# Performance work log

Hardware: AMD Instinct MI355X
Metric: run time of the kernel (lower is better)

Reference implementation:

```python
import jax, jax.numpy as jnp
import numpy as np

D_MODEL, D_KEY, N_HEADS = 256, 32, 8
B, T1, T2 = 4, 2048, 2048


def setup_inputs() -> dict:
    key = jax.random.key(0)
    ks = jax.random.split(key, 12)
    s = 1.0 / np.sqrt(D_MODEL)
    inp = {
        "key_input": jax.random.normal(ks[0], (B, T1, D_MODEL), jnp.float32),
        "query_input": jax.random.normal(ks[1], (B, T2, D_MODEL), jnp.float32),
        "value_input": jax.random.normal(ks[2], (B, T1, D_MODEL), jnp.float32),
        "attention_mask": jnp.ones((B, T1, T2), dtype=jnp.bool_),  # unused by the module, kept for API fidelity
        "WK_w": jax.random.uniform(ks[3], (D_KEY * N_HEADS, D_MODEL), jnp.float32, -s, s),
        "WK_b": jax.random.uniform(ks[4], (D_KEY * N_HEADS,), jnp.float32, -s, s),
        "WQ_w": jax.random.uniform(ks[5], (D_KEY * N_HEADS, D_MODEL), jnp.float32, -s, s),
        "WQ_b": jax.random.uniform(ks[6], (D_KEY * N_HEADS,), jnp.float32, -s, s),
        "WV_w": jax.random.uniform(ks[7], (D_MODEL * N_HEADS, D_MODEL), jnp.float32, -s, s),
        "WV_b": jax.random.uniform(ks[8], (D_MODEL * N_HEADS,), jnp.float32, -s, s),
        "WO_w": jax.random.uniform(ks[9], (D_MODEL, D_MODEL * N_HEADS), jnp.float32, -1.0 / np.sqrt(D_MODEL * N_HEADS), 1.0 / np.sqrt(D_MODEL * N_HEADS)),
        "WO_b": jax.random.uniform(ks[10], (D_MODEL,), jnp.float32, -1.0 / np.sqrt(D_MODEL * N_HEADS), 1.0 / np.sqrt(D_MODEL * N_HEADS)),
    }
    return inp


def reference(key_input, query_input, value_input, attention_mask,
              WK_w, WK_b, WQ_w, WQ_b, WV_w, WV_b, WO_w, WO_b):
    b, t1, dm = key_input.shape
    t2 = query_input.shape[1]
    h, dk = N_HEADS, D_KEY
    # projections
    k = key_input @ WK_w.T + WK_b      # [b, t1, h*dk]
    q = query_input @ WQ_w.T + WQ_b    # [b, t2, h*dk]
    v = value_input @ WV_w.T + WV_b    # [b, t1, h*dm] (per-head value dim == d_model)
    # head split: channel index c = head*dk + feat (head outer), matching torch reshapes
    k = k.reshape(b, t1, h, dk)
    q = q.reshape(b, t2, h, dk)
    v = v.reshape(b, t1, h, dm)
    # scores: NO 1/sqrt(dk) scaling and NO masking (faithful to source; mask arg unused)
    scores = jnp.einsum('bshk,bqhk->bhsq', k, q)      # [b, h, t1, t2]
    attn = jax.nn.softmax(scores, axis=2)             # softmax over KEY axis (torch dim=1 of [t1,t2])
    emb = jnp.einsum('bshd,bhsq->bqdh', v, attn)      # [b, t2, dm, h]
    emb = emb.reshape(b, t2, dm * h)                  # flatten (d_model outer, head inner)
    return emb @ WO_w.T + WO_b                        # [b, t2, d_model]
```

## Files before the change

### kernel.cpp

```cpp
#include <hip/hip_runtime.h>

typedef __attribute__((ext_vector_type(8))) short short8;
typedef __attribute__((ext_vector_type(4))) short short4v;
typedef __attribute__((ext_vector_type(4))) float float4v;
typedef __attribute__((ext_vector_type(4))) unsigned uint4v;
typedef __attribute__((ext_vector_type(2))) unsigned uint2v;
typedef __attribute__((ext_vector_type(4))) _Float16 half4;

constexpr int T  = 2048;
constexpr int DM = 256;
constexpr int DK = 32;

__device__ inline short f2bf(float f) {
  unsigned u = __builtin_bit_cast(unsigned, f);
  u += 0x7fff + ((u >> 16) & 1);
  return (short)(u >> 16);
}

__device__ inline unsigned pk2(float a, float b) {
#if __has_builtin(__builtin_amdgcn_cvt_pk_bf16_f32)
  auto r = __builtin_amdgcn_cvt_pk_bf16_f32(a, b);
  return __builtin_bit_cast(unsigned, r);
#else
  unsigned ua = __builtin_bit_cast(unsigned, a);
  ua = (ua + 0x7fff + ((ua >> 16) & 1)) >> 16;
  unsigned ub = __builtin_bit_cast(unsigned, b);
  ub = (ub + 0x7fff + ((ub >> 16) & 1)) >> 16;
  return ua | (ub << 16);
#endif
}

__device__ inline float fexp2(float x) {
#if __has_builtin(__builtin_amdgcn_exp2f)
  return __builtin_amdgcn_exp2f(x);
#else
  return exp2f(x);
#endif
}

__device__ inline short8 load8_bf(const float* __restrict__ p) {
  float4v a = *(const float4v*)p;
  float4v b = *(const float4v*)(p + 4);
  uint4v u;
  u[0] = pk2(a[0], a[1]); u[1] = pk2(a[2], a[3]);
  u[2] = pk2(b[0], b[1]); u[3] = pk2(b[2], b[3]);
  return __builtin_bit_cast(short8, u);
}

__device__ inline void gemm_body64(const float* __restrict__ A,
                                   const float* __restrict__ Bw,
                                   const float* __restrict__ bias,
                                   short* __restrict__ C,
                                   float oscale, int bx, int by,
                                   int K, int N,
                                   short (&As)[128][40], short (&Bs)[64][40]) {
  const int tid  = threadIdx.x;
  const int wave = tid >> 6, lane = tid & 63;
  const int l15  = lane & 15, quad = lane >> 4;
  const int wm   = (wave & 1) * 64, wn = (wave >> 1) * 32;
  const long Abase = (long)bx * 128;
  const long Bbase = (long)by * 64;

  float4v acc[4][2];
  for (int i = 0; i < 4; i++)
    for (int j = 0; j < 2; j++)
      for (int r = 0; r < 4; r++) acc[i][j][r] = 0.f;

  const int srow = tid >> 2;
  const int sc8  = (tid & 3) * 8;

  for (int k0 = 0; k0 < K; k0 += 32) {
    __syncthreads();
    for (int i = 0; i < 2; i++) {
      int row = srow + i * 64;
      *(short8*)&As[row][sc8] = load8_bf(A + (Abase + row) * K + k0 + sc8);
    }
    *(short8*)&Bs[srow][sc8] = load8_bf(Bw + (Bbase + srow) * K + k0 + sc8);
    __syncthreads();
    short8 af[4], bfr[2];
    for (int ms = 0; ms < 4; ms++) af[ms]  = *(const short8*)&As[wm + ms*16 + l15][quad*8];
    for (int ns = 0; ns < 2; ns++) bfr[ns] = *(const short8*)&Bs[wn + ns*16 + l15][quad*8];
    for (int ms = 0; ms < 4; ms++)
      for (int ns = 0; ns < 2; ns++)
        acc[ms][ns] = __builtin_amdgcn_mfma_f32_16x16x32_bf16(af[ms], bfr[ns], acc[ms][ns], 0, 0, 0);
  }

  for (int ms = 0; ms < 4; ms++) {
    int rowl = wm + ms*16 + quad*4;
    for (int ns = 0; ns < 2; ns++) {
      int col = (int)Bbase + wn + ns*16 + l15;
      float bv = bias[col];
      for (int r = 0; r < 4; r++) {
        long row = Abase + rowl + r;
        C[row * (long)N + col] = f2bf((acc[ms][ns][r] + bv) * oscale);
      }
    }
  }
}

__global__ __launch_bounds__(256)
void prep(const float* __restrict__ key_x, const float* __restrict__ query_x,
          const float* __restrict__ WK_w, const float* __restrict__ WK_b,
          const float* __restrict__ WQ_w, const float* __restrict__ WQ_b,
          const float* __restrict__ WV_w, const float* __restrict__ WV_b,
          const float* __restrict__ WO_w,
          short* __restrict__ Kp, short* __restrict__ Qp,
          short* __restrict__ Wf, float* __restrict__ cbias) {
  __shared__ __align__(16) short As[128][40];
  __shared__ __align__(16) short Bs[64][40];
  __shared__ float cb_s[16][17];

  const int gb  = blockIdx.x;
  const int tid = threadIdx.x;

  if (gb < 512) {
    const int g = gb & 255;
    const int bx = g & 63, by = g >> 6;
    if (gb < 256)
      gemm_body64(key_x,   WK_w, WK_b, Kp, 1.0f,        bx, by, 256, 256, As, Bs);
    else
      gemm_body64(query_x, WQ_w, WQ_b, Qp, 1.44269504f, bx, by, 256, 256, As, Bs);
  } else if (gb < 576) {
    const int w  = gb - 512;
    const int h  = w >> 3;
    const int bx = (w >> 2) & 1;
    const int by = w & 3;
    const int wave = tid >> 6, lane = tid & 63;
    const int l15  = lane & 15, quad = lane >> 4;
    const int wm   = (wave & 1) * 64, wn = (wave >> 1) * 32;
    const int srow = tid >> 2, sc8 = (tid & 3) * 8;

    float4v acc[4][2];
    for (int i = 0; i < 4; i++)
      for (int j = 0; j < 2; j++)
        for (int r = 0; r < 4; r++) acc[i][j][r] = 0.f;

    for (int d0 = 0; d0 < 256; d0 += 32) {
      __syncthreads();
      for (int i = 0; i < 2; i++) {
        int row = srow + i * 64;
        for (int j = 0; j < 8; j++)
          As[row][sc8 + j] = f2bf(WO_w[(bx*128 + row) * 2048 + (d0 + sc8 + j) * 8 + h]);
      }
      for (int j = 0; j < 8; j++)
        Bs[srow][sc8 + j] = f2bf(WV_w[((h*256) + d0 + sc8 + j) * 256 + by*64 + srow]);
      __syncthreads();
      short8 af[4], bfr[2];
      for (int ms = 0; ms < 4; ms++) af[ms]  = *(const short8*)&As[wm + ms*16 + l15][quad*8];
      for (int ns = 0; ns < 2; ns++) bfr[ns] = *(const short8*)&Bs[wn + ns*16 + l15][quad*8];
      for (int ms = 0; ms < 4; ms++)
        for (int ns = 0; ns < 2; ns++)
          acc[ms][ns] = __builtin_amdgcn_mfma_f32_16x16x32_bf16(af[ms], bfr[ns], acc[ms][ns], 0, 0, 0);
    }
    for (int ms = 0; ms < 4; ms++) {
      int m = bx*128 + wm + ms*16 + quad*4;
      for (int ns = 0; ns < 2; ns++) {
        int col = by*64 + wn + ns*16 + l15;
        for (int r = 0; r < 4; r++)
          Wf[((long)h*256 + m + r) * 256 + col] = f2bf(acc[ms][ns][r]);
      }
    }
  } else {
    const int idx = gb - 576;
    const int h = idx >> 4, ng = idx & 15;
    const int ni = tid & 15, di = tid >> 4;
    const int n = ng * 16 + ni;
    float acc = 0.f;
    for (int j = 0; j < 16; j++) {
      int d = di * 16 + j;
      acc += WV_b[h*256 + d] * WO_w[n * 2048 + d*8 + h];
    }
    cb_s[ni][di] = acc;
    __syncthreads();
    if (tid < 16) {
      float s = 0.f;
      for (int d2 = 0; d2 < 16; d2++) s += cb_s[tid][d2];
      cbias[h*256 + ng*16 + tid] = s;
    }
  }
}

__global__ __launch_bounds__(256)
void gemm_ut(const short* __restrict__ Wf, const float* __restrict__ Bw,
             const float* __restrict__ cbias, short* __restrict__ Ut) {
  __shared__ __align__(16) short As[128][40];
  __shared__ __align__(16) short Bs[128][40];

  const int tid  = threadIdx.x;
  const int wave = tid >> 6, lane = tid & 63;
  const int l15  = lane & 15, quad = lane >> 4;
  const int wm   = (wave & 1) * 64, wn = (wave >> 1) * 64;
  const long Abase = (long)blockIdx.x * 128;
  const long Bbase = (long)blockIdx.y * 128;

  float4v acc[4][4];
  for (int i = 0; i < 4; i++)
    for (int j = 0; j < 4; j++)
      for (int r = 0; r < 4; r++) acc[i][j][r] = 0.f;

  const int srow = tid >> 2;
  const int sc8  = (tid & 3) * 8;

  for (int k0 = 0; k0 < 256; k0 += 32) {
    __syncthreads();
    for (int i = 0; i < 2; i++) {
      int row = srow + i * 64;
      *(short8*)&As[row][sc8] = *(const short8*)(Wf + (Abase + row) * 256 + k0 + sc8);
      *(short8*)&Bs[row][sc8] = load8_bf(Bw + (Bbase + row) * 256 + k0 + sc8);
    }
    __syncthreads();
    short8 af[4], bfr[4];
    for (int ms = 0; ms < 4; ms++) af[ms]  = *(const short8*)&As[wm + ms*16 + l15][quad*8];
    for (int ns = 0; ns < 4; ns++) bfr[ns] = *(const short8*)&Bs[wn + ns*16 + l15][quad*8];
    for (int ms = 0; ms < 4; ms++)
      for (int ns = 0; ns < 4; ns++)
        acc[ms][ns] = __builtin_amdgcn_mfma_f32_16x16x32_bf16(af[ms], bfr[ns], acc[ms][ns], 0, 0, 0);
  }

  for (int ms = 0; ms < 4; ms++) {
    int rowl = wm + ms*16 + quad*4;
    for (int ns = 0; ns < 4; ns++) {
      int col = (int)Bbase + wn + ns*16 + l15;
      int bidx = col >> 11, scol = col & 2047;
      for (int r = 0; r < 4; r++) {
        long m = Abase + rowl + r;
        Ut[((long)bidx * 2048 + m) * 2048 + scol] = f2bf(acc[ms][ns][r] + cbias[m]);
      }
    }
  }
}

__global__ __launch_bounds__(256, 2)
void attn_kernel(const short* __restrict__ Kp, const short* __restrict__ Qp,
                 const short* __restrict__ Ut, _Float16* __restrict__ partial) {
  __shared__ __align__(16) short Pt[2][128][136];
  __shared__ __align__(16) float psum[128][4];

  const int tid  = threadIdx.x;
  const int wave = tid >> 6, lane = tid & 63;
  const int l15  = lane & 15, quad = lane >> 4;

  const int L  = blockIdx.x;
  const int h  = L & 7;
  const int b  = (L >> 3) & 3;
  const int q0 = (L >> 5) * 128;

  const short* Kbh = Kp + (long)b * T * DM + h * DK;
  const short* Qbh = Qp + (long)b * T * DM + h * DK;
  const short* Ubh = Ut + ((long)b * 2048 + h * 256) * 2048;

  float4v acc[4][8];
  for (int i = 0; i < 4; i++)
    for (int j = 0; j < 8; j++)
      for (int r = 0; r < 4; r++) acc[i][j][r] = 0.f;

  float ps[8];
  for (int i = 0; i < 8; i++) ps[i] = 0.f;

  short8 qf[8];
  for (int qs = 0; qs < 8; qs++)
    qf[qs] = *(const short8*)(Qbh + (long)(q0 + qs*16 + l15) * DM + quad*8);

  auto computeSt = [&](int s0, int buf) {
    for (int ss = 0; ss < 2; ss++) {
      short8 kf = *(const short8*)(Kbh + (long)(s0 + wave*32 + ss*16 + l15) * DM + quad*8);
      for (int qs = 0; qs < 8; qs++) {
        float4v z = {0.f, 0.f, 0.f, 0.f};
        float4v st = __builtin_amdgcn_mfma_f32_16x16x32_bf16(kf, qf[qs], z, 0, 0, 0);
        float p0 = fexp2(st[0]), p1 = fexp2(st[1]);
        float p2 = fexp2(st[2]), p3 = fexp2(st[3]);
        ps[qs] += (p0 + p1) + (p2 + p3);
        uint2v pb; pb[0] = pk2(p0, p1); pb[1] = pk2(p2, p3);
        *(uint2v*)&Pt[buf][qs*16 + l15][wave*32 + ss*16 + quad*4] = pb;
      }
    }
  };

  computeSt(0, 0);

  for (int it = 0; it < T / 128; it++) {
    const int buf = it & 1;
    const int s0  = it * 128;
    __syncthreads();
    if (it < T / 128 - 1) computeSt(s0 + 128, buf ^ 1);
    for (int ks = 0; ks < 4; ks++) {
      short8 pf[8];
      for (int ns = 0; ns < 8; ns++)
        pf[ns] = *(const short8*)&Pt[buf][ns*16 + l15][ks*32 + quad*8];
      for (int ms = 0; ms < 4; ms++) {
        short8 vf = *(const short8*)(Ubh + (long)(wave*64 + ms*16 + l15) * 2048
                                     + s0 + ks*32 + quad*8);
        for (int ns = 0; ns < 8; ns++)
          acc[ms][ns] = __builtin_amdgcn_mfma_f32_16x16x32_bf16(vf, pf[ns], acc[ms][ns], 0, 0, 0);
      }
    }
  }

  for (int qs = 0; qs < 8; qs++) {
    ps[qs] += __shfl_xor(ps[qs], 16, 64);
    ps[qs] += __shfl_xor(ps[qs], 32, 64);
  }
  if (lane < 16)
    for (int qs = 0; qs < 8; qs++) psum[qs*16 + lane][wave] = ps[qs];
  __syncthreads();

  for (int ns = 0; ns < 8; ns++) {
    float4v sv = *(const float4v*)&psum[ns*16 + l15][0];
    float rl = 1.0f / (sv[0] + sv[1] + sv[2] + sv[3]);
    long pbase = ((long)h * 8192 + b * T + q0 + ns*16 + l15) * 256;
    for (int ms = 0; ms < 4; ms++) {
      int ncol = wave*64 + ms*16 + quad*4;
      half4 hv;
      for (int r = 0; r < 4; r++) hv[r] = (_Float16)(acc[ms][ns][r] * rl);
      *(half4*)(partial + pbase + ncol) = hv;
    }
  }
}

__global__ void reduce_out(const _Float16* __restrict__ partial,
                           const float* __restrict__ WO_b,
                           float* __restrict__ out) {
  const long HP = 8192L * 256;
  long i4 = ((long)blockIdx.x * 256 + threadIdx.x) * 4;
  float4v o = *(const float4v*)(WO_b + (i4 & 255));
  for (int h = 0; h < 8; h++) {
    half4 hv = *(const half4*)(partial + h * HP + i4);
    for (int r = 0; r < 4; r++) o[r] += (float)hv[r];
  }
  *(float4v*)(out + i4) = o;
}

extern "C" void kernel_launch(void* const* d_in, const int* in_sizes, int n_in,
                              void* d_out, int out_size, void* d_ws, size_t ws_size,
                              hipStream_t stream) {
  const float* key_x   = (const float*)d_in[0];
  const float* query_x = (const float*)d_in[1];
  const float* value_x = (const float*)d_in[2];
  const float* WK_w = (const float*)d_in[4];
  const float* WK_b = (const float*)d_in[5];
  const float* WQ_w = (const float*)d_in[6];
  const float* WQ_b = (const float*)d_in[7];
  const float* WV_w = (const float*)d_in[8];
  const float* WV_b = (const float*)d_in[9];
  const float* WO_w = (const float*)d_in[10];
  const float* WO_b = (const float*)d_in[11];

  char* ws = (char*)d_ws;
  short*     Kp    = (short*)(ws);
  short*     Qp    = (short*)(ws + (4u  << 20));
  short*     Ut    = (short*)(ws + (8u  << 20));
  short*     Wf    = (short*)(ws + (40u << 20));
  float*     cbias = (float*)(ws + (41u << 20));
  _Float16*  part  = (_Float16*)(ws + (42u << 20));
  float*     outp  = (float*)d_out;

  prep<<<704, 256, 0, stream>>>(key_x, query_x, WK_w, WK_b, WQ_w, WQ_b,
                                WV_w, WV_b, WO_w, Kp, Qp, Wf, cbias);
  gemm_ut<<<dim3(16, 64), 256, 0, stream>>>(Wf, value_x, cbias, Ut);
  attn_kernel<<<dim3(512), 256, 0, stream>>>(Kp, Qp, Ut, part);
  reduce_out<<<2048, 256, 0, stream>>>(part, WO_b, outp);
}
```

Baseline: 295.7 us.

## Fuse all stages into one cooperative persistent kernel with grid syncs

Measured after the change: 402.6 us. +36.2%, slower.

```diff
diff --git a/kernel.cpp b/kernel.cpp
--- a/kernel.cpp
+++ b/kernel.cpp
@@ -1,4 +1,7 @@
 #include <hip/hip_runtime.h>
+#include <hip/hip_cooperative_groups.h>
+
+namespace cg = cooperative_groups;
 
 typedef __attribute__((ext_vector_type(8))) short short8;
 typedef __attribute__((ext_vector_type(4))) short short4v;
@@ -47,13 +50,14 @@
   return __builtin_bit_cast(short8, u);
 }
 
-__device__ inline void gemm_body64(const float* __restrict__ A,
-                                   const float* __restrict__ Bw,
-                                   const float* __restrict__ bias,
-                                   short* __restrict__ C,
-                                   float oscale, int bx, int by,
-                                   int K, int N,
-                                   short (&As)[128][40], short (&Bs)[64][40]) {
+
+__device__ inline void proj_body(const float* __restrict__ A,
+                                 const float* __restrict__ Bw,
+                                 const float* __restrict__ bias,
+                                 short* __restrict__ C, float oscale,
+                                 int bx, int by, char* smem) {
+  auto As = (short(*)[40])smem;
+  auto Bs = (short(*)[40])(smem + 10240);
   const int tid  = threadIdx.x;
   const int wave = tid >> 6, lane = tid & 63;
   const int l15  = lane & 15, quad = lane >> 4;
@@ -69,13 +73,13 @@
   const int srow = tid >> 2;
   const int sc8  = (tid & 3) * 8;
 
-  for (int k0 = 0; k0 < K; k0 += 32) {
+  for (int k0 = 0; k0 < 256; k0 += 32) {
     __syncthreads();
     for (int i = 0; i < 2; i++) {
       int row = srow + i * 64;
-      *(short8*)&As[row][sc8] = load8_bf(A + (Abase + row) * K + k0 + sc8);
-    }
-    *(short8*)&Bs[srow][sc8] = load8_bf(Bw + (Bbase + srow) * K + k0 + sc8);
+      *(short8*)&As[row][sc8] = load8_bf(A + (Abase + row) * 256 + k0 + sc8);
+    }
+    *(short8*)&Bs[srow][sc8] = load8_bf(Bw + (Bbase + srow) * 256 + k0 + sc8);
     __syncthreads();
     short8 af[4], bfr[2];
     for (int ms = 0; ms < 4; ms++) af[ms]  = *(const short8*)&As[wm + ms*16 + l15][quad*8];
@@ -92,106 +96,93 @@
       float bv = bias[col];
       for (int r = 0; r < 4; r++) {
         long row = Abase + rowl + r;
-        C[row * (long)N + col] = f2bf((acc[ms][ns][r] + bv) * oscale);
+        C[row * 256 + col] = f2bf((acc[ms][ns][r] + bv) * oscale);
       }
     }
   }
 }
 
-__global__ __launch_bounds__(256)
-void prep(const float* __restrict__ key_x, const float* __restrict__ query_x,
-          const float* __restrict__ WK_w, const float* __restrict__ WK_b,
-          const float* __restrict__ WQ_w, const float* __restrict__ WQ_b,
-          const float* __restrict__ WV_w, const float* __restrict__ WV_b,
-          const float* __restrict__ WO_w,
-          short* __restrict__ Kp, short* __restrict__ Qp,
-          short* __restrict__ Wf, float* __restrict__ cbias) {
-  __shared__ __align__(16) short As[128][40];
-  __shared__ __align__(16) short Bs[64][40];
-  __shared__ float cb_s[16][17];
-
-  const int gb  = blockIdx.x;
+__device__ inline void wf_body(const float* __restrict__ WO_w,
+                               const float* __restrict__ WV_w,
+                               short* __restrict__ Wf,
+                               int h, int bx, int by, char* smem) {
+  auto As = (short(*)[40])smem;
+  auto Bs = (short(*)[40])(smem + 10240);
+  const int tid  = threadIdx.x;
+  const int wave = tid >> 6, lane = tid & 63;
+  const int l15  = lane & 15, quad = lane >> 4;
+  const int wm   = (wave & 1) * 64, wn = (wave >> 1) * 32;
+  const int srow = tid >> 2, sc8 = (tid & 3) * 8;
+
+  float4v acc[4][2];
+  for (int i = 0; i < 4; i++)
+    for (int j = 0; j < 2; j++)
+      for (int r = 0; r < 4; r++) acc[i][j][r] = 0.f;
+
+  for (int d0 = 0; d0 < 256; d0 += 32) {
+    __syncthreads();
+    for (int i = 0; i < 2; i++) {
+      int row = srow + i * 64;
+      for (int j = 0; j < 8; j++)
+        As[row][sc8 + j] = f2bf(WO_w[(bx*128 + row) * 2048 + (d0 + sc8 + j) * 8 + h]);
+    }
+    for (int j = 0; j < 8; j++)
+      Bs[srow][sc8 + j] = f2bf(WV_w[((h*256) + d0 + sc8 + j) * 256 + by*64 + srow]);
+    __syncthreads();
+    short8 af[4], bfr[2];
+    for (int ms = 0; ms < 4; ms++) af[ms]  = *(const short8*)&As[wm + ms*16 + l15][quad*8];
+    for (int ns = 0; ns < 2; ns++) bfr[ns] = *(const short8*)&Bs[wn + ns*16 + l15][quad*8];
+    for (int ms = 0; ms < 4; ms++)
+      for (int ns = 0; ns < 2; ns++)
+        acc[ms][ns] = __builtin_amdgcn_mfma_f32_16x16x32_bf16(af[ms], bfr[ns], acc[ms][ns], 0, 0, 0);
+  }
+  for (int ms = 0; ms < 4; ms++) {
+    int m = bx*128 + wm + ms*16 + quad*4;
+    for (int ns = 0; ns < 2; ns++) {
+      int col = by*64 + wn + ns*16 + l15;
+      for (int r = 0; r < 4; r++)
+        Wf[((long)h*256 + m + r) * 256 + col] = f2bf(acc[ms][ns][r]);
+    }
+  }
+}
+
+__device__ inline void cbias_body(const float* __restrict__ WV_b,
+                                  const float* __restrict__ WO_w,
+                                  float* __restrict__ cbias,
+                                  int idx, char* smem) {
+  float* cb_s = (float*)smem;
   const int tid = threadIdx.x;
-
-  if (gb < 512) {
-    const int g = gb & 255;
-    const int bx = g & 63, by = g >> 6;
-    if (gb < 256)
-      gemm_body64(key_x,   WK_w, WK_b, Kp, 1.0f,        bx, by, 256, 256, As, Bs);
-    else
-      gemm_body64(query_x, WQ_w, WQ_b, Qp, 1.44269504f, bx, by, 256, 256, As, Bs);
-  } else if (gb < 576) {
-    const int w  = gb - 512;
-    const int h  = w >> 3;
-    const int bx = (w >> 2) & 1;
-    const int by = w & 3;
-    const int wave = tid >> 6, lane = tid & 63;
-    const int l15  = lane & 15, quad = lane >> 4;
-    const int wm   = (wave & 1) * 64, wn = (wave >> 1) * 32;
-    const int srow = tid >> 2, sc8 = (tid & 3) * 8;
-
-    float4v acc[4][2];
-    for (int i = 0; i < 4; i++)
-      for (int j = 0; j < 2; j++)
-        for (int r = 0; r < 4; r++) acc[i][j][r] = 0.f;
-
-    for (int d0 = 0; d0 < 256; d0 += 32) {
-      __syncthreads();
-      for (int i = 0; i < 2; i++) {
-        int row = srow + i * 64;
-        for (int j = 0; j < 8; j++)
-          As[row][sc8 + j] = f2bf(WO_w[(bx*128 + row) * 2048 + (d0 + sc8 + j) * 8 + h]);
-      }
-      for (int j = 0; j < 8; j++)
-        Bs[srow][sc8 + j] = f2bf(WV_w[((h*256) + d0 + sc8 + j) * 256 + by*64 + srow]);
-      __syncthreads();
-      short8 af[4], bfr[2];
-      for (int ms = 0; ms < 4; ms++) af[ms]  = *(const short8*)&As[wm + ms*16 + l15][quad*8];
-      for (int ns = 0; ns < 2; ns++) bfr[ns] = *(const short8*)&Bs[wn + ns*16 + l15][quad*8];
-      for (int ms = 0; ms < 4; ms++)
-        for (int ns = 0; ns < 2; ns++)
-          acc[ms][ns] = __builtin_amdgcn_mfma_f32_16x16x32_bf16(af[ms], bfr[ns], acc[ms][ns], 0, 0, 0);
-    }
-    for (int ms = 0; ms < 4; ms++) {
-      int m = bx*128 + wm + ms*16 + quad*4;
-      for (int ns = 0; ns < 2; ns++) {
-        int col = by*64 + wn + ns*16 + l15;
-        for (int r = 0; r < 4; r++)
-          Wf[((long)h*256 + m + r) * 256 + col] = f2bf(acc[ms][ns][r]);
-      }
-    }
-  } else {
-    const int idx = gb - 576;
-    const int h = idx >> 4, ng = idx & 15;
-    const int ni = tid & 15, di = tid >> 4;
-    const int n = ng * 16 + ni;
-    float acc = 0.f;
-    for (int j = 0; j < 16; j++) {
-      int d = di * 16 + j;
-      acc += WV_b[h*256 + d] * WO_w[n * 2048 + d*8 + h];
-    }
-    cb_s[ni][di] = acc;
-    __syncthreads();
-    if (tid < 16) {
-      float s = 0.f;
-      for (int d2 = 0; d2 < 16; d2++) s += cb_s[tid][d2];
-      cbias[h*256 + ng*16 + tid] = s;
-    }
-  }
-}
-
-__global__ __launch_bounds__(256)
-void gemm_ut(const short* __restrict__ Wf, const float* __restrict__ Bw,
-             const float* __restrict__ cbias, short* __restrict__ Ut) {
-  __shared__ __align__(16) short As[128][40];
-  __shared__ __align__(16) short Bs[128][40];
-
+  const int h = idx >> 4, ng = idx & 15;
+  const int ni = tid & 15, di = tid >> 4;
+  const int n = ng * 16 + ni;
+  float acc = 0.f;
+  for (int j = 0; j < 16; j++) {
+    int d = di * 16 + j;
+    acc += WV_b[h*256 + d] * WO_w[n * 2048 + d*8 + h];
+  }
+  cb_s[ni*17 + di] = acc;
+  __syncthreads();
+  if (tid < 16) {
+    float s = 0.f;
+    for (int d2 = 0; d2 < 16; d2++) s += cb_s[tid*17 + d2];
+    cbias[h*256 + ng*16 + tid] = s;
+  }
+  __syncthreads();
+}
+
+__device__ inline void ut_body(const short* __restrict__ Wf,
+                               const float* __restrict__ Bw,
+                               const float* __restrict__ cbias,
+                               short* __restrict__ Ut,
+                               int bx, int by, char* smem) {
+  auto As = (short(*)[40])smem;
+  auto Bs = (short(*)[40])(smem + 10240);
   const int tid  = threadIdx.x;
   const int wave = tid >> 6, lane = tid & 63;
   const int l15  = lane & 15, quad = lane >> 4;
   const int wm   = (wave & 1) * 64, wn = (wave >> 1) * 64;
-  const long Abase = (long)blockIdx.x * 128;
-  const long Bbase = (long)blockIdx.y * 128;
+  const long Abase = (long)bx * 128;
+  const long Bbase = (long)by * 128;
 
   float4v acc[4][4];
   for (int i = 0; i < 4; i++)
@@ -230,17 +221,19 @@
   }
 }
 
-__global__ __launch_bounds__(256, 2)
-void attn_kernel(const short* __restrict__ Kp, const short* __restrict__ Qp,
-                 const short* __restrict__ Ut, _Float16* __restrict__ partial) {
-  __shared__ __align__(16) short Pt[2][128][136];
-  __shared__ __align__(16) float psum[128][4];
+__device__ inline void attn_body(const short* __restrict__ Kp,
+                                 const short* __restrict__ Qp,
+                                 const short* __restrict__ Ut,
+                                 _Float16* __restrict__ partial,
+                                 int L, char* smem) {
+  typedef short PtRow[136];
+  PtRow* Pt   = (PtRow*)smem;
+  float* psum = (float*)(smem + 2*128*136*2);
 
   const int tid  = threadIdx.x;
   const int wave = tid >> 6, lane = tid & 63;
   const int l15  = lane & 15, quad = lane >> 4;
 
-  const int L  = blockIdx.x;
   const int h  = L & 7;
   const int b  = (L >> 3) & 3;
   const int q0 = (L >> 5) * 128;
@@ -271,7 +264,7 @@
         float p2 = fexp2(st[2]), p3 = fexp2(st[3]);
         ps[qs] += (p0 + p1) + (p2 + p3);
         uint2v pb; pb[0] = pk2(p0, p1); pb[1] = pk2(p2, p3);
-        *(uint2v*)&Pt[buf][qs*16 + l15][wave*32 + ss*16 + quad*4] = pb;
+        *(uint2v*)&Pt[buf*128 + qs*16 + l15][wave*32 + ss*16 + quad*4] = pb;
       }
     }
   };
@@ -286,7 +279,7 @@
     for (int ks = 0; ks < 4; ks++) {
       short8 pf[8];
       for (int ns = 0; ns < 8; ns++)
-        pf[ns] = *(const short8*)&Pt[buf][ns*16 + l15][ks*32 + quad*8];
+        pf[ns] = *(const short8*)&Pt[buf*128 + ns*16 + l15][ks*32 + quad*8];
       for (int ms = 0; ms < 4; ms++) {
         short8 vf = *(const short8*)(Ubh + (long)(wave*64 + ms*16 + l15) * 2048
                                      + s0 + ks*32 + quad*8);
@@ -301,11 +294,11 @@
     ps[qs] += __shfl_xor(ps[qs], 32, 64);
   }
   if (lane < 16)
-    for (int qs = 0; qs < 8; qs++) psum[qs*16 + lane][wave] = ps[qs];
+    for (int qs = 0; qs < 8; qs++) psum[(qs*16 + lane)*4 + wave] = ps[qs];
   __syncthreads();
 
   for (int ns = 0; ns < 8; ns++) {
-    float4v sv = *(const float4v*)&psum[ns*16 + l15][0];
+    float4v sv = *(const float4v*)&psum[(ns*16 + l15)*4];
     float rl = 1.0f / (sv[0] + sv[1] + sv[2] + sv[3]);
     long pbase = ((long)h * 8192 + b * T + q0 + ns*16 + l15) * 256;
     for (int ms = 0; ms < 4; ms++) {
@@ -317,9 +310,93 @@
   }
 }
 
-__global__ void reduce_out(const _Float16* __restrict__ partial,
-                           const float* __restrict__ WO_b,
-                           float* __restrict__ out) {
+__global__ __launch_bounds__(256, 2)
+void mega(const float* __restrict__ key_x, const float* __restrict__ query_x,
+          const float* __restrict__ value_x,
+          const float* __restrict__ WK_w, const float* __restrict__ WK_b,
+          const float* __restrict__ WQ_w, const float* __restrict__ WQ_b,
+          const float* __restrict__ WV_w, const float* __restrict__ WV_b,
+          const float* __restrict__ WO_w, const float* __restrict__ WO_b,
+          short* __restrict__ Kp, short* __restrict__ Qp,
+          short* __restrict__ Ut, short* __restrict__ Wf,
+          float* __restrict__ cbias, _Float16* __restrict__ part,
+          float* __restrict__ outp) {
+  __shared__ __align__(16) char smem[71680];
+  cg::grid_group grid = cg::this_grid();
+  const int gb = blockIdx.x;
+
+  if (gb < 256)
+    proj_body(key_x, WK_w, WK_b, Kp, 1.0f, gb & 63, gb >> 6, smem);
+  else
+    proj_body(query_x, WQ_w, WQ_b, Qp, 1.44269504f, (gb - 256) & 63, (gb - 256) >> 6, smem);
+  __syncthreads();
+  if (gb < 64)
+    wf_body(WO_w, WV_w, Wf, gb >> 3, (gb >> 2) & 1, gb & 3, smem);
+  else if (gb < 192)
+    cbias_body(WV_b, WO_w, cbias, gb - 64, smem);
+
+  __threadfence();
+  grid.sync();
+
+  for (int jj = gb; jj < 1024; jj += 512)
+    ut_body(Wf, value_x, cbias, Ut, jj & 15, jj >> 4, smem);
+
+  __threadfence();
+  grid.sync();
+
+  attn_body(Kp, Qp, Ut, part, gb, smem);
+
+  __threadfence();
+  grid.sync();
+
+  {
+    const long HP = 8192L * 256;
+    for (int it = 0; it < 4; it++) {
+      long i4 = ((long)gb * 1024 + it * 256 + threadIdx.x) * 4;
+      float4v o = *(const float4v*)(WO_b + (i4 & 255));
+      for (int h = 0; h < 8; h++) {
+        half4 hv = *(const half4*)(part + h * HP + i4);
+        for (int r = 0; r < 4; r++) o[r] += (float)hv[r];
+      }
+      *(float4v*)(outp + i4) = o;
+    }
+  }
+}
+
+__global__ __launch_bounds__(256)
+void prep_k(const float* key_x, const float* query_x,
+            const float* WK_w, const float* WK_b,
+            const float* WQ_w, const float* WQ_b,
+            const float* WV_w, const float* WV_b, const float* WO_w,
+            short* Kp, short* Qp, short* Wf, float* cbias) {
+  __shared__ __align__(16) char smem[15360];
+  const int gb = blockIdx.x;
+  if (gb < 256)
+    proj_body(key_x, WK_w, WK_b, Kp, 1.0f, gb & 63, gb >> 6, smem);
+  else if (gb < 512)
+    proj_body(query_x, WQ_w, WQ_b, Qp, 1.44269504f, (gb - 256) & 63, (gb - 256) >> 6, smem);
+  else if (gb < 576) {
+    int w = gb - 512;
+    wf_body(WO_w, WV_w, Wf, w >> 3, (w >> 2) & 1, w & 3, smem);
+  } else
+    cbias_body(WV_b, WO_w, cbias, gb - 576, smem);
+}
+
+__global__ __launch_bounds__(256)
+void ut_k(const short* Wf, const float* Bw, const float* cbias, short* Ut) {
+  __shared__ __align__(16) char smem[20480];
+  ut_body(Wf, Bw, cbias, Ut, blockIdx.x, blockIdx.y, smem);
+}
+
+__global__ __launch_bounds__(256, 2)
+void attn_k(const short* Kp, const short* Qp, const short* Ut, _Float16* part) {
+  __shared__ __align__(16) char smem[71680];
+  attn_body(Kp, Qp, Ut, part, blockIdx.x, smem);
+}
+
+__global__ void reduce_k(const _Float16* __restrict__ partial,
+                         const float* __restrict__ WO_b,
+                         float* __restrict__ out) {
   const long HP = 8192L * 256;
   long i4 = ((long)blockIdx.x * 256 + threadIdx.x) * 4;
   float4v o = *(const float4v*)(WO_b + (i4 & 255));
@@ -354,9 +431,26 @@
   _Float16*  part  = (_Float16*)(ws + (42u << 20));
   float*     outp  = (float*)d_out;
 
-  prep<<<704, 256, 0, stream>>>(key_x, query_x, WK_w, WK_b, WQ_w, WQ_b,
-                                WV_w, WV_b, WO_w, Kp, Qp, Wf, cbias);
-  gemm_ut<<<dim3(16, 64), 256, 0, stream>>>(Wf, value_x, cbias, Ut);
-  attn_kernel<<<dim3(512), 256, 0, stream>>>(Kp, Qp, Ut, part);
-  reduce_out<<<2048, 256, 0, stream>>>(part, WO_b, outp);
-}
+  int nb = 0;
+  hipError_t qe = hipOccupancyMaxActiveBlocksPerMultiprocessor(&nb, mega, 256, 0);
+  bool done = false;
+  if (qe == hipSuccess && nb >= 2) {
+    void* args[] = {
+      (void*)&key_x, (void*)&query_x, (void*)&value_x,
+      (void*)&WK_w, (void*)&WK_b, (void*)&WQ_w, (void*)&WQ_b,
+      (void*)&WV_w, (void*)&WV_b, (void*)&WO_w, (void*)&WO_b,
+      (void*)&Kp, (void*)&Qp, (void*)&Ut, (void*)&Wf,
+      (void*)&cbias, (void*)&part, (void*)&outp
+    };
+    hipError_t e = hipLaunchCooperativeKernel((const void*)mega, dim3(512),
+                                              dim3(256), args, 0, stream);
+    done = (e == hipSuccess);
+  }
+  if (!done) {
+    prep_k<<<704, 256, 0, stream>>>(key_x, query_x, WK_w, WK_b, WQ_w, WQ_b,
+                                    WV_w, WV_b, WO_w, Kp, Qp, Wf, cbias);
+    ut_k<<<dim3(16, 64), 256, 0, stream>>>(Wf, value_x, cbias, Ut);
+    attn_k<<<512, 256, 0, stream>>>(Kp, Qp, Ut, part);
+    reduce_k<<<2048, 256, 0, stream>>>(part, WO_b, outp);
+  }
+}
```

## Regroup launches so K/Q projections share a kernel with the Ut GEMM

Applied to the files above, without the earlier changes.

Result: slower. 304.1 us (+2.8%).

```diff
diff --git a/kernel.cpp b/kernel.cpp
--- a/kernel.cpp
+++ b/kernel.cpp
@@ -47,13 +47,13 @@
   return __builtin_bit_cast(short8, u);
 }
 
-__device__ inline void gemm_body64(const float* __restrict__ A,
-                                   const float* __restrict__ Bw,
-                                   const float* __restrict__ bias,
-                                   short* __restrict__ C,
-                                   float oscale, int bx, int by,
-                                   int K, int N,
-                                   short (&As)[128][40], short (&Bs)[64][40]) {
+
+__device__ inline void proj_body(const float* __restrict__ A,
+                                 const float* __restrict__ Bw,
+                                 const float* __restrict__ bias,
+                                 short* __restrict__ C, float oscale,
+                                 int bx, int by,
+                                 short (&As)[128][40], short (&Bs)[128][40]) {
   const int tid  = threadIdx.x;
   const int wave = tid >> 6, lane = tid & 63;
   const int l15  = lane & 15, quad = lane >> 4;
@@ -69,13 +69,13 @@
   const int srow = tid >> 2;
   const int sc8  = (tid & 3) * 8;
 
-  for (int k0 = 0; k0 < K; k0 += 32) {
+  for (int k0 = 0; k0 < 256; k0 += 32) {
     __syncthreads();
     for (int i = 0; i < 2; i++) {
       int row = srow + i * 64;
-      *(short8*)&As[row][sc8] = load8_bf(A + (Abase + row) * K + k0 + sc8);
-    }
-    *(short8*)&Bs[srow][sc8] = load8_bf(Bw + (Bbase + srow) * K + k0 + sc8);
+      *(short8*)&As[row][sc8] = load8_bf(A + (Abase + row) * 256 + k0 + sc8);
+    }
+    *(short8*)&Bs[srow][sc8] = load8_bf(Bw + (Bbase + srow) * 256 + k0 + sc8);
     __syncthreads();
     short8 af[4], bfr[2];
     for (int ms = 0; ms < 4; ms++) af[ms]  = *(const short8*)&As[wm + ms*16 + l15][quad*8];
@@ -92,106 +92,67 @@
       float bv = bias[col];
       for (int r = 0; r < 4; r++) {
         long row = Abase + rowl + r;
-        C[row * (long)N + col] = f2bf((acc[ms][ns][r] + bv) * oscale);
+        C[row * 256 + col] = f2bf((acc[ms][ns][r] + bv) * oscale);
       }
     }
   }
 }
 
-__global__ __launch_bounds__(256)
-void prep(const float* __restrict__ key_x, const float* __restrict__ query_x,
-          const float* __restrict__ WK_w, const float* __restrict__ WK_b,
-          const float* __restrict__ WQ_w, const float* __restrict__ WQ_b,
-          const float* __restrict__ WV_w, const float* __restrict__ WV_b,
-          const float* __restrict__ WO_w,
-          short* __restrict__ Kp, short* __restrict__ Qp,
-          short* __restrict__ Wf, float* __restrict__ cbias) {
-  __shared__ __align__(16) short As[128][40];
-  __shared__ __align__(16) short Bs[64][40];
-  __shared__ float cb_s[16][17];
-
-  const int gb  = blockIdx.x;
-  const int tid = threadIdx.x;
-
-  if (gb < 512) {
-    const int g = gb & 255;
-    const int bx = g & 63, by = g >> 6;
-    if (gb < 256)
-      gemm_body64(key_x,   WK_w, WK_b, Kp, 1.0f,        bx, by, 256, 256, As, Bs);
-    else
-      gemm_body64(query_x, WQ_w, WQ_b, Qp, 1.44269504f, bx, by, 256, 256, As, Bs);
-  } else if (gb < 576) {
-    const int w  = gb - 512;
-    const int h  = w >> 3;
-    const int bx = (w >> 2) & 1;
-    const int by = w & 3;
-    const int wave = tid >> 6, lane = tid & 63;
-    const int l15  = lane & 15, quad = lane >> 4;
-    const int wm   = (wave & 1) * 64, wn = (wave >> 1) * 32;
-    const int srow = tid >> 2, sc8 = (tid & 3) * 8;
-
-    float4v acc[4][2];
-    for (int i = 0; i < 4; i++)
-      for (int j = 0; j < 2; j++)
-        for (int r = 0; r < 4; r++) acc[i][j][r] = 0.f;
-
-    for (int d0 = 0; d0 < 256; d0 += 32) {
-      __syncthreads();
-      for (int i = 0; i < 2; i++) {
-        int row = srow + i * 64;
-        for (int j = 0; j < 8; j++)
-          As[row][sc8 + j] = f2bf(WO_w[(bx*128 + row) * 2048 + (d0 + sc8 + j) * 8 + h]);
-      }
+__device__ inline void wf_body(const float* __restrict__ WO_w,
+                               const float* __restrict__ WV_w,
+                               short* __restrict__ Wf,
+                               int h, int bx, int by,
+                               short (&As)[128][40], short (&Bs)[128][40]) {
+  const int tid  = threadIdx.x;
+  const int wave = tid >> 6, lane = tid & 63;
+  const int l15  = lane & 15, quad = lane >> 4;
+  const int wm   = (wave & 1) * 64, wn = (wave >> 1) * 32;
+  const int srow = tid >> 2, sc8 = (tid & 3) * 8;
+
+  float4v acc[4][2];
+  for (int i = 0; i < 4; i++)
+    for (int j = 0; j < 2; j++)
+      for (int r = 0; r < 4; r++) acc[i][j][r] = 0.f;
+
+  for (int d0 = 0; d0 < 256; d0 += 32) {
+    __syncthreads();
+    for (int i = 0; i < 2; i++) {
+      int row = srow + i * 64;
       for (int j = 0; j < 8; j++)
-        Bs[srow][sc8 + j] = f2bf(WV_w[((h*256) + d0 + sc8 + j) * 256 + by*64 + srow]);
-      __syncthreads();
-      short8 af[4], bfr[2];
-      for (int ms = 0; ms < 4; ms++) af[ms]  = *(const short8*)&As[wm + ms*16 + l15][quad*8];
-      for (int ns = 0; ns < 2; ns++) bfr[ns] = *(const short8*)&Bs[wn + ns*16 + l15][quad*8];
-      for (int ms = 0; ms < 4; ms++)
-        for (int ns = 0; ns < 2; ns++)
-          acc[ms][ns] = __builtin_amdgcn_mfma_f32_16x16x32_bf16(af[ms], bfr[ns], acc[ms][ns], 0, 0, 0);
-    }
-    for (int ms = 0; ms < 4; ms++) {
-      int m = bx*128 + wm + ms*16 + quad*4;
-      for (int ns = 0; ns < 2; ns++) {
-        int col = by*64 + wn + ns*16 + l15;
-        for (int r = 0; r < 4; r++)
-          Wf[((long)h*256 + m + r) * 256 + col] = f2bf(acc[ms][ns][r]);
-      }
-    }
-  } else {
-    const int idx = gb - 576;
-    const int h = idx >> 4, ng = idx & 15;
-    const int ni = tid & 15, di = tid >> 4;
-    const int n = ng * 16 + ni;
-    float acc = 0.f;
-    for (int j = 0; j < 16; j++) {
-      int d = di * 16 + j;
-      acc += WV_b[h*256 + d] * WO_w[n * 2048 + d*8 + h];
-    }
-    cb_s[ni][di] = acc;
-    __syncthreads();
-    if (tid < 16) {
-      float s = 0.f;
-      for (int d2 = 0; d2 < 16; d2++) s += cb_s[tid][d2];
-      cbias[h*256 + ng*16 + tid] = s;
-    }
-  }
-}
-
-__global__ __launch_bounds__(256)
-void gemm_ut(const short* __restrict__ Wf, const float* __restrict__ Bw,
-             const float* __restrict__ cbias, short* __restrict__ Ut) {
-  __shared__ __align__(16) short As[128][40];
-  __shared__ __align__(16) short Bs[128][40];
-
+        As[row][sc8 + j] = f2bf(WO_w[(bx*128 + row) * 2048 + (d0 + sc8 + j) * 8 + h]);
+    }
+    for (int j = 0; j < 8; j++)
+      Bs[srow][sc8 + j] = f2bf(WV_w[((h*256) + d0 + sc8 + j) * 256 + by*64 + srow]);
+    __syncthreads();
+    short8 af[4], bfr[2];
+    for (int ms = 0; ms < 4; ms++) af[ms]  = *(const short8*)&As[wm + ms*16 + l15][quad*8];
+    for (int ns = 0; ns < 2; ns++) bfr[ns] = *(const short8*)&Bs[wn + ns*16 + l15][quad*8];
+    for (int ms = 0; ms < 4; ms++)
+      for (int ns = 0; ns < 2; ns++)
+        acc[ms][ns] = __builtin_amdgcn_mfma_f32_16x16x32_bf16(af[ms], bfr[ns], acc[ms][ns], 0, 0, 0);
+  }
+  for (int ms = 0; ms < 4; ms++) {
+    int m = bx*128 + wm + ms*16 + quad*4;
+    for (int ns = 0; ns < 2; ns++) {
+      int col = by*64 + wn + ns*16 + l15;
+      for (int r = 0; r < 4; r++)
+        Wf[((long)h*256 + m + r) * 256 + col] = f2bf(acc[ms][ns][r]);
+    }
+  }
+}
+
+__device__ inline void ut_body(const short* __restrict__ Wf,
+                               const float* __restrict__ Bw,
+                               const float* __restrict__ cbias,
+                               short* __restrict__ Ut,
+                               int bx, int by,
+                               short (&As)[128][40], short (&Bs)[128][40]) {
   const int tid  = threadIdx.x;
   const int wave = tid >> 6, lane = tid & 63;
   const int l15  = lane & 15, quad = lane >> 4;
   const int wm   = (wave & 1) * 64, wn = (wave >> 1) * 64;
-  const long Abase = (long)blockIdx.x * 128;
-  const long Bbase = (long)blockIdx.y * 128;
+  const long Abase = (long)bx * 128;
+  const long Bbase = (long)by * 128;
 
   float4v acc[4][4];
   for (int i = 0; i < 4; i++)
@@ -227,6 +188,61 @@
         Ut[((long)bidx * 2048 + m) * 2048 + scol] = f2bf(acc[ms][ns][r] + cbias[m]);
       }
     }
+  }
+}
+
+__global__ __launch_bounds__(256)
+void prep1(const float* __restrict__ WV_w, const float* __restrict__ WV_b,
+           const float* __restrict__ WO_w,
+           short* __restrict__ Wf, float* __restrict__ cbias) {
+  __shared__ __align__(16) short As[128][40];
+  __shared__ __align__(16) short Bs[128][40];
+  __shared__ float cb_s[16][17];
+  const int gb  = blockIdx.x;
+  const int tid = threadIdx.x;
+
+  if (gb < 64) {
+    wf_body(WO_w, WV_w, Wf, gb >> 3, (gb >> 2) & 1, gb & 3, As, Bs);
+  } else {
+    const int idx = gb - 64;
+    const int h = idx >> 4, ng = idx & 15;
+    const int ni = tid & 15, di = tid >> 4;
+    const int n = ng * 16 + ni;
+    float acc = 0.f;
+    for (int j = 0; j < 16; j++) {
+      int d = di * 16 + j;
+      acc += WV_b[h*256 + d] * WO_w[n * 2048 + d*8 + h];
+    }
+    cb_s[ni][di] = acc;
+    __syncthreads();
+    if (tid < 16) {
+      float s = 0.f;
+      for (int d2 = 0; d2 < 16; d2++) s += cb_s[tid][d2];
+      cbias[h*256 + ng*16 + tid] = s;
+    }
+  }
+}
+
+__global__ __launch_bounds__(256)
+void front(const float* __restrict__ key_x, const float* __restrict__ query_x,
+           const float* __restrict__ value_x,
+           const float* __restrict__ WK_w, const float* __restrict__ WK_b,
+           const float* __restrict__ WQ_w, const float* __restrict__ WQ_b,
+           const short* __restrict__ Wf, const float* __restrict__ cbias,
+           short* __restrict__ Kp, short* __restrict__ Qp,
+           short* __restrict__ Ut) {
+  __shared__ __align__(16) short As[128][40];
+  __shared__ __align__(16) short Bs[128][40];
+  const int gb = blockIdx.x;
+
+  if (gb < 1024) {
+    ut_body(Wf, value_x, cbias, Ut, gb & 15, gb >> 4, As, Bs);
+  } else if (gb < 1280) {
+    const int g = gb - 1024;
+    proj_body(key_x, WK_w, WK_b, Kp, 1.0f, g & 63, g >> 6, As, Bs);
+  } else {
+    const int g = gb - 1280;
+    proj_body(query_x, WQ_w, WQ_b, Qp, 1.44269504f, g & 63, g >> 6, As, Bs);
   }
 }
 
@@ -354,9 +370,10 @@
   _Float16*  part  = (_Float16*)(ws + (42u << 20));
   float*     outp  = (float*)d_out;
 
-  prep<<<704, 256, 0, stream>>>(key_x, query_x, WK_w, WK_b, WQ_w, WQ_b,
-                                WV_w, WV_b, WO_w, Kp, Qp, Wf, cbias);
-  gemm_ut<<<dim3(16, 64), 256, 0, stream>>>(Wf, value_x, cbias, Ut);
-  attn_kernel<<<dim3(512), 256, 0, stream>>>(Kp, Qp, Ut, part);
+  prep1<<<192, 256, 0, stream>>>(WV_w, WV_b, WO_w, Wf, cbias);
+  front<<<1536, 256, 0, stream>>>(key_x, query_x, value_x,
+                                  WK_w, WK_b, WQ_w, WQ_b,
+                                  Wf, cbias, Kp, Qp, Ut);
+  attn_kernel<<<512, 256, 0, stream>>>(Kp, Qp, Ut, part);
   reduce_out<<<2048, 256, 0, stream>>>(part, WO_b, outp);
 }
```

## Pre-convert inputs to bf16 and merge K/Q projections into the Ut GEMM launch

Applied to the files above, without the earlier changes.

Result: no change. 298.7 us (+1.0%).

```diff
diff --git a/kernel.cpp b/kernel.cpp
--- a/kernel.cpp
+++ b/kernel.cpp
@@ -38,90 +38,44 @@
 #endif
 }
 
-__device__ inline short8 load8_bf(const float* __restrict__ p) {
-  float4v a = *(const float4v*)p;
-  float4v b = *(const float4v*)(p + 4);
-  uint4v u;
-  u[0] = pk2(a[0], a[1]); u[1] = pk2(a[2], a[3]);
-  u[2] = pk2(b[0], b[1]); u[3] = pk2(b[2], b[3]);
-  return __builtin_bit_cast(short8, u);
-}
-
-__device__ inline void gemm_body64(const float* __restrict__ A,
-                                   const float* __restrict__ Bw,
-                                   const float* __restrict__ bias,
-                                   short* __restrict__ C,
-                                   float oscale, int bx, int by,
-                                   int K, int N,
-                                   short (&As)[128][40], short (&Bs)[64][40]) {
-  const int tid  = threadIdx.x;
-  const int wave = tid >> 6, lane = tid & 63;
-  const int l15  = lane & 15, quad = lane >> 4;
-  const int wm   = (wave & 1) * 64, wn = (wave >> 1) * 32;
-  const long Abase = (long)bx * 128;
-  const long Bbase = (long)by * 64;
-
-  float4v acc[4][2];
-  for (int i = 0; i < 4; i++)
-    for (int j = 0; j < 2; j++)
-      for (int r = 0; r < 4; r++) acc[i][j][r] = 0.f;
-
-  const int srow = tid >> 2;
-  const int sc8  = (tid & 3) * 8;
-
-  for (int k0 = 0; k0 < K; k0 += 32) {
-    __syncthreads();
-    for (int i = 0; i < 2; i++) {
-      int row = srow + i * 64;
-      *(short8*)&As[row][sc8] = load8_bf(A + (Abase + row) * K + k0 + sc8);
-    }
-    *(short8*)&Bs[srow][sc8] = load8_bf(Bw + (Bbase + srow) * K + k0 + sc8);
-    __syncthreads();
-    short8 af[4], bfr[2];
-    for (int ms = 0; ms < 4; ms++) af[ms]  = *(const short8*)&As[wm + ms*16 + l15][quad*8];
-    for (int ns = 0; ns < 2; ns++) bfr[ns] = *(const short8*)&Bs[wn + ns*16 + l15][quad*8];
-    for (int ms = 0; ms < 4; ms++)
-      for (int ns = 0; ns < 2; ns++)
-        acc[ms][ns] = __builtin_amdgcn_mfma_f32_16x16x32_bf16(af[ms], bfr[ns], acc[ms][ns], 0, 0, 0);
-  }
-
-  for (int ms = 0; ms < 4; ms++) {
-    int rowl = wm + ms*16 + quad*4;
-    for (int ns = 0; ns < 2; ns++) {
-      int col = (int)Bbase + wn + ns*16 + l15;
-      float bv = bias[col];
-      for (int r = 0; r < 4; r++) {
-        long row = Abase + rowl + r;
-        C[row * (long)N + col] = f2bf((acc[ms][ns][r] + bv) * oscale);
-      }
-    }
+__device__ inline void conv_block(const float* __restrict__ src,
+                                  short* __restrict__ dst, int blk) {
+  const int tid = threadIdx.x;
+  for (int j = 0; j < 8; j++) {
+    int idx = blk * 8192 + j * 1024 + tid * 4;
+    float4v v = *(const float4v*)(src + idx);
+    uint2v u; u[0] = pk2(v[0], v[1]); u[1] = pk2(v[2], v[3]);
+    *(uint2v*)(dst + idx) = u;
   }
 }
 
 __global__ __launch_bounds__(256)
 void prep(const float* __restrict__ key_x, const float* __restrict__ query_x,
-          const float* __restrict__ WK_w, const float* __restrict__ WK_b,
-          const float* __restrict__ WQ_w, const float* __restrict__ WQ_b,
+          const float* __restrict__ value_x,
+          const float* __restrict__ WK_w, const float* __restrict__ WQ_w,
           const float* __restrict__ WV_w, const float* __restrict__ WV_b,
           const float* __restrict__ WO_w,
-          short* __restrict__ Kp, short* __restrict__ Qp,
+          short* __restrict__ Kb, short* __restrict__ Qb, short* __restrict__ Vb,
+          short* __restrict__ WKb, short* __restrict__ WQb,
           short* __restrict__ Wf, float* __restrict__ cbias) {
   __shared__ __align__(16) short As[128][40];
-  __shared__ __align__(16) short Bs[64][40];
+  __shared__ __align__(16) short Bs[128][40];
   __shared__ float cb_s[16][17];
-
   const int gb  = blockIdx.x;
   const int tid = threadIdx.x;
 
-  if (gb < 512) {
-    const int g = gb & 255;
-    const int bx = g & 63, by = g >> 6;
-    if (gb < 256)
-      gemm_body64(key_x,   WK_w, WK_b, Kp, 1.0f,        bx, by, 256, 256, As, Bs);
-    else
-      gemm_body64(query_x, WQ_w, WQ_b, Qp, 1.44269504f, bx, by, 256, 256, As, Bs);
-  } else if (gb < 576) {
-    const int w  = gb - 512;
+  if (gb < 256) {
+    conv_block(key_x, Kb, gb);
+  } else if (gb < 512) {
+    conv_block(query_x, Qb, gb - 256);
+  } else if (gb < 768) {
+    conv_block(value_x, Vb, gb - 512);
+  } else if (gb < 776) {
+    conv_block(WK_w, WKb, gb - 768);
+  } else if (gb < 784) {
+    conv_block(WQ_w, WQb, gb - 776);
+  } else if (gb < 848) {
+    const int w  = gb - 784;
     const int h  = w >> 3;
     const int bx = (w >> 2) & 1;
     const int by = w & 3;
@@ -161,7 +115,7 @@
       }
     }
   } else {
-    const int idx = gb - 576;
+    const int idx = gb - 848;
     const int h = idx >> 4, ng = idx & 15;
     const int ni = tid & 15, di = tid >> 4;
     const int n = ng * 16 + ni;
@@ -181,50 +135,108 @@
 }
 
 __global__ __launch_bounds__(256)
-void gemm_ut(const short* __restrict__ Wf, const float* __restrict__ Bw,
-             const float* __restrict__ cbias, short* __restrict__ Ut) {
-  __shared__ __align__(16) short As[128][40];
+void front(const short* __restrict__ Kb, const short* __restrict__ Qb,
+           const short* __restrict__ Vb,
+           const short* __restrict__ WKb, const short* __restrict__ WQb,
+           const float* __restrict__ WK_b, const float* __restrict__ WQ_b,
+           const short* __restrict__ Wf, const float* __restrict__ cbias,
+           short* __restrict__ Kp, short* __restrict__ Qp,
+           short* __restrict__ Ut) {
+  __shared__ __align__(16) short As[256][40];
   __shared__ __align__(16) short Bs[128][40];
-
-  const int tid  = threadIdx.x;
+  const int gb  = blockIdx.x;
+  const int tid = threadIdx.x;
   const int wave = tid >> 6, lane = tid & 63;
   const int l15  = lane & 15, quad = lane >> 4;
-  const int wm   = (wave & 1) * 64, wn = (wave >> 1) * 64;
-  const long Abase = (long)blockIdx.x * 128;
-  const long Bbase = (long)blockIdx.y * 128;
-
-  float4v acc[4][4];
-  for (int i = 0; i < 4; i++)
-    for (int j = 0; j < 4; j++)
-      for (int r = 0; r < 4; r++) acc[i][j][r] = 0.f;
-
   const int srow = tid >> 2;
   const int sc8  = (tid & 3) * 8;
 
-  for (int k0 = 0; k0 < 256; k0 += 32) {
-    __syncthreads();
-    for (int i = 0; i < 2; i++) {
-      int row = srow + i * 64;
-      *(short8*)&As[row][sc8] = *(const short8*)(Wf + (Abase + row) * 256 + k0 + sc8);
-      *(short8*)&Bs[row][sc8] = load8_bf(Bw + (Bbase + row) * 256 + k0 + sc8);
-    }
-    __syncthreads();
-    short8 af[4], bfr[4];
-    for (int ms = 0; ms < 4; ms++) af[ms]  = *(const short8*)&As[wm + ms*16 + l15][quad*8];
-    for (int ns = 0; ns < 4; ns++) bfr[ns] = *(const short8*)&Bs[wn + ns*16 + l15][quad*8];
-    for (int ms = 0; ms < 4; ms++)
-      for (int ns = 0; ns < 4; ns++)
-        acc[ms][ns] = __builtin_amdgcn_mfma_f32_16x16x32_bf16(af[ms], bfr[ns], acc[ms][ns], 0, 0, 0);
-  }
-
-  for (int ms = 0; ms < 4; ms++) {
-    int rowl = wm + ms*16 + quad*4;
-    for (int ns = 0; ns < 4; ns++) {
-      int col = (int)Bbase + wn + ns*16 + l15;
-      int bidx = col >> 11, scol = col & 2047;
-      for (int r = 0; r < 4; r++) {
-        long m = Abase + rowl + r;
-        Ut[((long)bidx * 2048 + m) * 2048 + scol] = f2bf(acc[ms][ns][r] + cbias[m]);
+  if (gb < 512) {
+    const int bx = gb & 7;
+    const int by = gb >> 3;
+    const long Abase = (long)bx * 256;
+    const long Bbase = (long)by * 128;
+
+    float4v acc[4][8];
+    for (int i = 0; i < 4; i++)
+      for (int j = 0; j < 8; j++)
+        for (int r = 0; r < 4; r++) acc[i][j][r] = 0.f;
+
+    for (int k0 = 0; k0 < 256; k0 += 32) {
+      __syncthreads();
+      for (int i = 0; i < 4; i++) {
+        int row = srow + i * 64;
+        *(short8*)&As[row][sc8] = *(const short8*)(Wf + (Abase + row) * 256 + k0 + sc8);
+      }
+      for (int i = 0; i < 2; i++) {
+        int row = srow + i * 64;
+        *(short8*)&Bs[row][sc8] = *(const short8*)(Vb + (Bbase + row) * 256 + k0 + sc8);
+      }
+      __syncthreads();
+      short8 af[4], bfr[8];
+      for (int ms = 0; ms < 4; ms++)
+        af[ms] = *(const short8*)&As[wave*64 + ms*16 + l15][quad*8];
+      for (int ns = 0; ns < 8; ns++)
+        bfr[ns] = *(const short8*)&Bs[ns*16 + l15][quad*8];
+      for (int ms = 0; ms < 4; ms++)
+        for (int ns = 0; ns < 8; ns++)
+          acc[ms][ns] = __builtin_amdgcn_mfma_f32_16x16x32_bf16(af[ms], bfr[ns], acc[ms][ns], 0, 0, 0);
+    }
+
+    for (int ms = 0; ms < 4; ms++) {
+      for (int ns = 0; ns < 8; ns++) {
+        int col = (int)Bbase + ns*16 + l15;
+        int bidx = col >> 11, scol = col & 2047;
+        for (int r = 0; r < 4; r++) {
+          long m = Abase + wave*64 + ms*16 + quad*4 + r;
+          Ut[((long)bidx * 2048 + m) * 2048 + scol] = f2bf(acc[ms][ns][r] + cbias[m]);
+        }
+      }
+    }
+  } else {
+    const bool isQ = (gb >= 768);
+    const int g   = gb - (isQ ? 768 : 512);
+    const int bx  = g & 63, by = g >> 6;
+    const short* A  = isQ ? Qb  : Kb;
+    const short* Bw = isQ ? WQb : WKb;
+    const float* bias = isQ ? WQ_b : WK_b;
+    short* C = isQ ? Qp : Kp;
+    const float oscale = isQ ? 1.44269504f : 1.0f;
+
+    const int wm = (wave & 1) * 64, wn = (wave >> 1) * 32;
+    const long Abase = (long)bx * 128;
+    const long Bbase = (long)by * 64;
+
+    float4v acc[4][2];
+    for (int i = 0; i < 4; i++)
+      for (int j = 0; j < 2; j++)
+        for (int r = 0; r < 4; r++) acc[i][j][r] = 0.f;
+
+    for (int k0 = 0; k0 < 256; k0 += 32) {
+      __syncthreads();
+      for (int i = 0; i < 2; i++) {
+        int row = srow + i * 64;
+        *(short8*)&As[row][sc8] = *(const short8*)(A + (Abase + row) * 256 + k0 + sc8);
+      }
+      *(short8*)&Bs[srow][sc8] = *(const short8*)(Bw + (Bbase + srow) * 256 + k0 + sc8);
+      __syncthreads();
+      short8 af[4], bfr[2];
+      for (int ms = 0; ms < 4; ms++) af[ms]  = *(const short8*)&As[wm + ms*16 + l15][quad*8];
+      for (int ns = 0; ns < 2; ns++) bfr[ns] = *(const short8*)&Bs[wn + ns*16 + l15][quad*8];
+      for (int ms = 0; ms < 4; ms++)
+        for (int ns = 0; ns < 2; ns++)
+          acc[ms][ns] = __builtin_amdgcn_mfma_f32_16x16x32_bf16(af[ms], bfr[ns], acc[ms][ns], 0, 0, 0);
+    }
+
+    for (int ms = 0; ms < 4; ms++) {
+      int rowl = wm + ms*16 + quad*4;
+      for (int ns = 0; ns < 2; ns++) {
+        int col = (int)Bbase + wn + ns*16 + l15;
+        float bv = bias[col];
+        for (int r = 0; r < 4; r++) {
+          long row = Abase + rowl + r;
+          C[row * 256 + col] = f2bf((acc[ms][ns][r] + bv) * oscale);
+        }
       }
     }
   }
@@ -351,12 +363,19 @@
   short*     Ut    = (short*)(ws + (8u  << 20));
   short*     Wf    = (short*)(ws + (40u << 20));
   float*     cbias = (float*)(ws + (41u << 20));
+  short*     Kb    = (short*)(ws + (42u << 20));
+  short*     Qb    = (short*)(ws + (46u << 20));
+  short*     Vb    = (short*)(ws + (50u << 20));
+  short*     WKb   = (short*)(ws + (54u << 20));
+  short*     WQb   = (short*)(ws + (54u << 20) + (128u << 10));
   _Float16*  part  = (_Float16*)(ws + (42u << 20));
   float*     outp  = (float*)d_out;
 
-  prep<<<704, 256, 0, stream>>>(key_x, query_x, WK_w, WK_b, WQ_w, WQ_b,
-                                WV_w, WV_b, WO_w, Kp, Qp, Wf, cbias);
-  gemm_ut<<<dim3(16, 64), 256, 0, stream>>>(Wf, value_x, cbias, Ut);
-  attn_kernel<<<dim3(512), 256, 0, stream>>>(Kp, Qp, Ut, part);
+  prep<<<976, 256, 0, stream>>>(key_x, query_x, value_x, WK_w, WQ_w,
+                                WV_w, WV_b, WO_w,
+                                Kb, Qb, Vb, WKb, WQb, Wf, cbias);
+  front<<<1024, 256, 0, stream>>>(Kb, Qb, Vb, WKb, WQb, WK_b, WQ_b,
+                                  Wf, cbias, Kp, Qp, Ut);
+  attn_kernel<<<512, 256, 0, stream>>>(Kp, Qp, Ut, part);
   reduce_out<<<2048, 256, 0, stream>>>(part, WO_b, outp);
 }
```
